# Performance work log

Hardware: AMD Instinct MI355X
Metric: run time of the kernel (lower is better)

Reference implementation:

```python
import jax, jax.numpy as jnp
import numpy as np

B, IN_DIM, HID, SUB_IN, SUB_OUT, GRID = 4096, 256, 512, 256, 256, 32
LN_EPS = 1e-5


def setup_inputs() -> dict:
    key = jax.random.key(0)
    ks = jax.random.split(key, 16)
    inp = {
        'x':  jax.random.normal(ks[0], (B, IN_DIM), jnp.float32),
        'h0': jax.random.normal(ks[1], (B, HID), jnp.float32),
        'c0': jax.random.normal(ks[2], (B, HID), jnp.float32),
        's0': jax.random.normal(ks[3], (B, SUB_OUT), jnp.float32),
        # LSTM gate params
        'kernel':  jax.random.normal(ks[4], (IN_DIM, 3 * HID), jnp.float32) * 0.05,
        'rkernel': jax.random.normal(ks[5], (HID, 3 * HID), jnp.float32) * 0.05,
        'bias':    jnp.zeros((3 * HID,), jnp.float32),
        # sub-layer recurrent mixing kernels (num_sub_layers=1)
        'sub_kx': jax.random.normal(ks[6], (1, IN_DIM, SUB_IN), jnp.float32) * 0.05,
        'sub_kh': jax.random.normal(ks[7], (1, SUB_OUT, SUB_IN), jnp.float32) * 0.05,
        'sub_tkan_kernel': jax.random.normal(ks[8], (1, 2 * SUB_OUT), jnp.float32) * 0.05,
        # Fourier KAN coefficients: (2, outdim, indim, gridsize) + bias
        'fc': jax.random.normal(ks[9], (2, SUB_OUT, SUB_IN, GRID), jnp.float32) / np.sqrt(SUB_IN * GRID),
        'fb': jnp.zeros((SUB_OUT,), jnp.float32),
        # aggregation + layer norm
        'agg_w': jax.random.normal(ks[10], (SUB_OUT, HID), jnp.float32) * 0.05,
        'agg_b': jnp.zeros((HID,), jnp.float32),
        'ln_g':  jnp.ones((HID,), jnp.float32),
        'ln_b':  jnp.zeros((HID,), jnp.float32),
    }
    return inp


def _fourier_kan(z, fc, fb):
    # z: [B, SUB_IN] -> [B, SUB_OUT]
    k = jnp.arange(1, GRID + 1, dtype=z.dtype)          # [G]
    ang = z[:, :, None] * k                             # [B, IN, G]
    return (jnp.einsum('big,oig->bo', jnp.cos(ang), fc[0])
            + jnp.einsum('big,oig->bo', jnp.sin(ang), fc[1]) + fb)


def reference(x, h0, c0, s0, kernel, rkernel, bias, sub_kx, sub_kh,
              sub_tkan_kernel, fc, fb, agg_w, agg_b, ln_g, ln_b):
    # LSTM-style gates (note: candidate also passes through sigmoid then tanh,
    # exactly as in the torch source)
    gates = jax.nn.sigmoid(x @ kernel + h0 @ rkernel + bias)      # [B, 3H]
    i, f, c_cand = jnp.split(gates, 3, axis=-1)
    c = f * c0 + i * jnp.tanh(c_cand)                             # [B, H]

    # single KAN sub-layer
    agg_in = x @ sub_kx[0] + s0 @ sub_kh[0]                       # [B, SUB_IN]
    sub_out = _fourier_kan(agg_in, fc, fb)                        # [B, SUB_OUT]
    rk_h, rk_x = jnp.split(sub_tkan_kernel[0], 2)                 # [SUB_OUT] each
    new_s = rk_h * sub_out + s0 * rk_x

    # aggregation -> output gate
    o = jax.nn.sigmoid(sub_out @ agg_w + agg_b)                   # [B, H]
    h = o * jnp.tanh(c)

    # layer norm
    mu = jnp.mean(h, axis=-1, keepdims=True)
    var = jnp.mean(jnp.square(h - mu), axis=-1, keepdims=True)
    h = (h - mu) * jax.lax.rsqrt(var + LN_EPS) * ln_g + ln_b
    return (h, c, new_s)
```

## Files before the change

kernel.cpp:

```cpp
#include <hip/hip_runtime.h>
#include <hip/hip_bf16.h>

typedef __bf16 bf16_t;
typedef __bf16 bf16x4 __attribute__((ext_vector_type(4)));
typedef __bf16 bf16x8 __attribute__((ext_vector_type(8)));
typedef float  f32x4  __attribute__((ext_vector_type(4)));

#define NB 4096
#define IN_DIM 256
#define HID 512
#define SUB 256
#define GRID_ 32

__device__ __forceinline__ float fract_f(float x) {
#if __has_builtin(__builtin_amdgcn_fractf)
  return __builtin_amdgcn_fractf(x);
#else
  return x - floorf(x);
#endif
}
__device__ __forceinline__ float cos_rev(float rev) {
#if __has_builtin(__builtin_amdgcn_cosf)
  return __builtin_amdgcn_cosf(rev);
#else
  return __cosf(rev * 6.283185307179586f);
#endif
}
__device__ __forceinline__ float sin_rev(float rev) {
#if __has_builtin(__builtin_amdgcn_sinf)
  return __builtin_amdgcn_sinf(rev);
#else
  return __sinf(rev * 6.283185307179586f);
#endif
}
__device__ __forceinline__ float sigm(float v) { return 1.f / (1.f + __expf(-v)); }
__device__ __forceinline__ float fast_tanh(float x) {
  float e = __expf(2.f * x);
  return (e - 1.f) / (e + 1.f);
}
#define INV2PI 0.15915494309189535f

#define O_XHI   0ull
#define O_XLO   2097152ull
#define O_H0    4194304ull
#define O_S0H   8388608ull
#define O_S0L   10485760ull
#define O_FCB   12582912ull
#define O_O     12582912ull
#define O_KT    20971520ull
#define O_RKT   21757952ull
#define O_AWT   23330816ull
#define O_KXH   23592960ull
#define O_KXL   23724032ull
#define O_KHH   23855104ull
#define O_KHL   23986176ull
#define O_TC    24117248ull
#define O_SOB   32505856ull
#define O_AGG   34603008ull
#define O_P3    38797312ull

__device__ __forceinline__ void tconv_body(const float* __restrict__ src,
                                           bf16_t* __restrict__ hi,
                                           bf16_t* __restrict__ lo,
                                           int R, int C, int bx, int by,
                                           bool wantlo, float scale) {
  __shared__ float t[32][33];
  int c0 = bx * 32, r0 = by * 32;
  int tx = threadIdx.x & 31, ty = threadIdx.x >> 5;
#pragma unroll
  for (int rr = 0; rr < 4; rr++) {
    int r = ty + rr * 8;
    t[r][tx] = src[(size_t)(r0 + r) * C + c0 + tx];
  }
  __syncthreads();
#pragma unroll
  for (int rr = 0; rr < 4; rr++) {
    int cl = ty + rr * 8;
    float f = t[tx][cl] * scale;
    bf16_t h = (bf16_t)f;
    size_t oi = (size_t)(c0 + cl) * R + r0 + tx;
    hi[oi] = h;
    if (wantlo) lo[oi] = (bf16_t)(f - (float)h);
  }
}

__global__ __launch_bounds__(256) void k_prep(const float* __restrict__ x,
                                              const float* __restrict__ h0,
                                              const float* __restrict__ s0,
                                              const float* __restrict__ fc,
                                              const float* __restrict__ Wk,
                                              const float* __restrict__ Wr,
                                              const float* __restrict__ aw,
                                              const float* __restrict__ kx,
                                              const float* __restrict__ kh,
                                              bf16_t* __restrict__ xhi, bf16_t* __restrict__ xlo,
                                              bf16_t* __restrict__ h0b,
                                              bf16_t* __restrict__ s0h, bf16_t* __restrict__ s0l,
                                              bf16_t* __restrict__ fcb2,
                                              bf16_t* __restrict__ kt,
                                              bf16_t* __restrict__ rkt,
                                              bf16_t* __restrict__ awt,
                                              bf16_t* __restrict__ kxh, bf16_t* __restrict__ kxl,
                                              bf16_t* __restrict__ khh, bf16_t* __restrict__ khl) {
  int bid = blockIdx.x;
  if (bid < 2048) {
    for (int q = bid * 256 + threadIdx.x; q < 2097152; q += 524288) {
      if (q < 1048576) {
        const float* src; bf16_t* hi; bf16_t* lo = nullptr; int base;
        if (q < 262144)       { src = x;  hi = xhi; lo = xlo; base = q; }
        else if (q < 786432)  { src = h0; hi = h0b;           base = q - 262144; }
        else                  { src = s0; hi = s0h; lo = s0l; base = q - 786432; }
        float4 v = *(const float4*)(src + (size_t)base * 4);
        bf16x4 h; h[0] = (bf16_t)v.x; h[1] = (bf16_t)v.y; h[2] = (bf16_t)v.z; h[3] = (bf16_t)v.w;
        *(bf16x4*)(hi + (size_t)base * 4) = h;
        if (lo) {
          bf16x4 l;
          l[0] = (bf16_t)(v.x - (float)h[0]); l[1] = (bf16_t)(v.y - (float)h[1]);
          l[2] = (bf16_t)(v.z - (float)h[2]); l[3] = (bf16_t)(v.w - (float)h[3]);
          *(bf16x4*)(lo + (size_t)base * 4) = l;
        }
      } else {
        int f = q - 1048576;
        int e = f * 4;
        int g = e & 31, i = (e >> 5) & 255, o = (e >> 13) & 255, s = e >> 21;
        float4 v = *(const float4*)(fc + (size_t)e);
        bf16x4 h; h[0] = (bf16_t)v.x; h[1] = (bf16_t)v.y; h[2] = (bf16_t)v.z; h[3] = (bf16_t)v.w;
        int nb = o >> 7, wn = (o >> 6) & 1, j = (o >> 4) & 3, lr = o & 15;
        int g4 = g >> 3, t0 = g & 7;
        size_t idx = ((((((size_t)(i * 2 + nb) * 2 + wn) * 4 + j) * 2 + s) * 4 + g4) * 16 + lr) * 8 + t0;
        *(bf16x4*)(fcb2 + idx) = h;
      }
    }
  } else {
    int b = bid - 2048;
    if (b < 384)       { tconv_body(Wk, kt,  nullptr, 256, 1536, b % 48, b / 48, false, 1.f); }
    else if (b < 1152) { b -= 384;  tconv_body(Wr, rkt, nullptr, 512, 1536, b % 48, b / 48, false, 1.f); }
    else if (b < 1280) { b -= 1152; tconv_body(aw, awt, nullptr, 256, 512,  b % 16, b / 16, false, 1.f); }
    else if (b < 1344) { b -= 1280; tconv_body(kx, kxh, kxl,     256, 256,  b % 8,  b / 8,  true, INV2PI); }
    else               { b -= 1344; tconv_body(kh, khh, khl,     256, 256,  b % 8,  b / 8,  true, INV2PI); }
  }
}

struct Pass { const bf16_t* A; const bf16_t* Bt; int K; int lda; int ldbt; };
struct GArgs {
  Pass p[6]; int np;
  const float* bias;
  int act;
  float* out; int ldout;
};

template<int BM, int BN>
__global__ __launch_bounds__(512) void k_gemm(GArgs g) {
  constexpr int MI = BM / 32;
  constexpr int NJ = BN / 64;
  constexpr int IA = (BM * 8) / 512;
  constexpr int IB = (BN * 8) / 512;
  __shared__ bf16_t smA[BM * 64];
  __shared__ bf16_t smB[BN * 64];
  const int tid = threadIdx.x;
  const int m0 = blockIdx.y * BM, n0 = blockIdx.x * BN;
  const int wv = tid >> 6, lane = tid & 63;
  const int wm = wv >> 2, wn = wv & 3;
  const int lr = lane & 15, g4 = lane >> 4;

  f32x4 acc[MI][NJ];
#pragma unroll
  for (int i = 0; i < MI; i++)
#pragma unroll
    for (int j = 0; j < NJ; j++) acc[i][j] = f32x4{0.f, 0.f, 0.f, 0.f};

  for (int ps = 0; ps < g.np; ps++) {
    const bf16_t* A = g.p[ps].A;
    const bf16_t* Bt = g.p[ps].Bt;
    const int K = g.p[ps].K, lda = g.p[ps].lda, ldbt = g.p[ps].ldbt;
    for (int k0 = 0; k0 < K; k0 += 64) {
      bf16x8 ar[IA], br[IB];
#pragma unroll
      for (int r = 0; r < IA; r++) {
        int task = tid + r * 512, row = task >> 3, t = task & 7, sf = t ^ (row & 7);
        ar[r] = *(const bf16x8*)(A + (size_t)(m0 + row) * lda + k0 + sf * 8);
      }
#pragma unroll
      for (int r = 0; r < IB; r++) {
        int task = tid + r * 512, row = task >> 3, t = task & 7, sf = t ^ (row & 7);
        br[r] = *(const bf16x8*)(Bt + (size_t)(n0 + row) * ldbt + k0 + sf * 8);
      }
      __syncthreads();
#pragma unroll
      for (int r = 0; r < IA; r++) {
        int task = tid + r * 512, row = task >> 3, t = task & 7;
        *(bf16x8*)(smA + row * 64 + t * 8) = ar[r];
      }
#pragma unroll
      for (int r = 0; r < IB; r++) {
        int task = tid + r * 512, row = task >> 3, t = task & 7;
        *(bf16x8*)(smB + row * 64 + t * 8) = br[r];
      }
      __syncthreads();
#pragma unroll
      for (int ks = 0; ks < 2; ks++) {
        bf16x8 af[MI], bfr[NJ];
#pragma unroll
        for (int i = 0; i < MI; i++) {
          int row = wm * (BM / 2) + i * 16 + lr;
          af[i] = *(const bf16x8*)(smA + row * 64 + ((ks * 4 + g4) ^ (lr & 7)) * 8);
        }
#pragma unroll
        for (int j = 0; j < NJ; j++) {
          int row = wn * (BN / 4) + j * 16 + lr;
          bfr[j] = *(const bf16x8*)(smB + row * 64 + ((ks * 4 + g4) ^ (lr & 7)) * 8);
        }
#pragma unroll
        for (int i = 0; i < MI; i++)
#pragma unroll
          for (int j = 0; j < NJ; j++)
            acc[i][j] = __builtin_amdgcn_mfma_f32_16x16x32_bf16(af[i], bfr[j], acc[i][j], 0, 0, 0);
      }
    }
  }
#pragma unroll
  for (int i = 0; i < MI; i++)
#pragma unroll
    for (int j = 0; j < NJ; j++) {
      int col = n0 + wn * (BN / 4) + j * 16 + lr;
      float bb = g.bias ? g.bias[col] : 0.f;
#pragma unroll
      for (int r = 0; r < 4; r++) {
        int row = m0 + wm * (BM / 2) + i * 16 + (lane >> 4) * 4 + r;
        float v = acc[i][j][r] + bb;
        if (g.act == 1) v = sigm(v);
        g.out[(size_t)row * g.ldout + col] = v;
      }
    }
}

struct GatesArgs {
  const bf16_t* xhi; const bf16_t* h0b; const bf16_t* kt; const bf16_t* rkt;
  const float* bias; const float* c0; float* c_out; float* tc;
};

__global__ __launch_bounds__(512, 2) void k_gates(GatesArgs ga) {
  __shared__ bf16_t smA[64 * 64];
  __shared__ bf16_t smB[3 * 128 * 64];
  const int tid = threadIdx.x;
  const int n0 = blockIdx.x * 128;
  const int m0 = blockIdx.y * 64;
  const int wv = tid >> 6, lane = tid & 63;
  const int wm = wv >> 2, wn = wv & 3;
  const int lr = lane & 15, g4 = lane >> 4;

  f32x4 acc[3][2][2];
#pragma unroll
  for (int t = 0; t < 3; t++)
#pragma unroll
    for (int i = 0; i < 2; i++)
#pragma unroll
      for (int j = 0; j < 2; j++) acc[t][i][j] = f32x4{0.f, 0.f, 0.f, 0.f};

  for (int ps = 0; ps < 2; ps++) {
    const bf16_t* A  = ps ? ga.h0b : ga.xhi;
    const bf16_t* Bt = ps ? ga.rkt : ga.kt;
    const int K = ps ? 512 : 256, ld = K;
    for (int k0 = 0; k0 < K; k0 += 64) {
      int arow = tid >> 3, at = tid & 7, asf = at ^ (arow & 7);
      bf16x8 ar = *(const bf16x8*)(A + (size_t)(m0 + arow) * ld + k0 + asf * 8);
      bf16x8 br[6];
#pragma unroll
      for (int r = 0; r < 6; r++) {
        int task = tid + r * 512;
        int gate = task >> 10, rem = task & 1023, o = rem >> 3, t = rem & 7, sf = t ^ (o & 7);
        br[r] = *(const bf16x8*)(Bt + (size_t)(gate * 512 + n0 + o) * ld + k0 + sf * 8);
      }
      __syncthreads();
      *(bf16x8*)(smA + arow * 64 + at * 8) = ar;
#pragma unroll
      for (int r = 0; r < 6; r++) {
        int task = tid + r * 512;
        int gate = task >> 10, rem = task & 1023, o = rem >> 3, t = rem & 7;
        *(bf16x8*)(smB + (gate * 128 + o) * 64 + t * 8) = br[r];
      }
      __syncthreads();
#pragma unroll
      for (int ks = 0; ks < 2; ks++) {
        bf16x8 af[2];
#pragma unroll
        for (int i = 0; i < 2; i++) {
          int row = wm * 32 + i * 16 + lr;
          af[i] = *(const bf16x8*)(smA + row * 64 + ((ks * 4 + g4) ^ (lr & 7)) * 8);
        }
#pragma unroll
        for (int t = 0; t < 3; t++) {
          bf16x8 bfr[2];
#pragma unroll
          for (int j = 0; j < 2; j++) {
            int row = wn * 32 + j * 16 + lr;
            bfr[j] = *(const bf16x8*)(smB + (t * 128 + row) * 64 + ((ks * 4 + g4) ^ (lr & 7)) * 8);
          }
#pragma unroll
          for (int i = 0; i < 2; i++)
#pragma unroll
            for (int j = 0; j < 2; j++)
              acc[t][i][j] = __builtin_amdgcn_mfma_f32_16x16x32_bf16(af[i], bfr[j], acc[t][i][j], 0, 0, 0);
        }
      }
    }
  }
#pragma unroll
  for (int i = 0; i < 2; i++)
#pragma unroll
    for (int j = 0; j < 2; j++) {
      int col = n0 + wn * 32 + j * 16 + lr;
      float bi = ga.bias[col], bf_ = ga.bias[512 + col], bc = ga.bias[1024 + col];
#pragma unroll
      for (int r = 0; r < 4; r++) {
        int row = m0 + wm * 32 + i * 16 + (lane >> 4) * 4 + r;
        size_t idx = (size_t)row * 512 + col;
        float iv = sigm(acc[0][i][j][r] + bi);
        float fv = sigm(acc[1][i][j][r] + bf_);
        float cc = sigm(acc[2][i][j][r] + bc);
        float cv = fv * ga.c0[idx] + iv * fast_tanh(cc);
        ga.c_out[idx] = cv;
        ga.tc[idx] = fast_tanh(cv);
      }
    }
}

struct FArgs { const float* agg; const bf16_t* fcb2; float* P[8]; };

__global__ __launch_bounds__(256, 2) void k_fourier(FArgs fa) {
  __shared__ float  zl[128 * 33];
  __shared__ bf16_t Asm[2][128 * 64];
  const int tid = threadIdx.x;
  const int bx = blockIdx.x;
  const int q = bx & 7, nb = (bx >> 3) & 1, mb = bx >> 4;
  const int m0 = mb * 128, n0 = nb * 128, i0 = q * 32;
  const int wv = tid >> 6, lane = tid & 63;
  const int wm = wv >> 1, wn = wv & 1;
  const int lr = lane & 15, g4 = lane >> 4;

#pragma unroll
  for (int r = 0; r < 4; r++) {
    int task = tid + r * 256, row = task >> 3, seg = task & 7;
    float4 v = *(const float4*)(fa.agg + (size_t)(m0 + row) * 256 + i0 + seg * 4);
    zl[row * 33 + seg * 4 + 0] = v.x;
    zl[row * 33 + seg * 4 + 1] = v.y;
    zl[row * 33 + seg * 4 + 2] = v.z;
    zl[row * 33 + seg * 4 + 3] = v.w;
  }

  const bf16_t* pB = fa.fcb2 + (size_t)i0 * 16384 + nb * 8192 + wn * 4096 + lane * 8;
  auto loadB = [&](int i, bf16x8 (&b)[8]) {
#pragma unroll
    for (int ks = 0; ks < 2; ks++)
#pragma unroll
      for (int j = 0; j < 4; j++)
        b[ks * 4 + j] = *(const bf16x8*)(pB + (size_t)i * 16384 + j * 1024 + ks * 512);
  };

  const int grow = tid >> 1, hp = tid & 1;
  const float* zp = zl + grow * 33;
  const int as0 = grow * 64 + (((2 * hp    ) ^ (grow & 7)) * 8);
  const int as1 = grow * 64 + (((2 * hp + 1) ^ (grow & 7)) * 8);
  const int as2 = grow * 64 + (((4 + 2 * hp) ^ (grow & 7)) * 8);
  const int as3 = grow * 64 + (((5 + 2 * hp) ^ (grow & 7)) * 8);
  auto genA = [&](int i, bf16_t* Ab) {
    float zr = zp[i];
    bf16x8 c0v, c1v, s0v, s1v;
#pragma unroll
    for (int t = 0; t < 8; t++) {
      float r0 = fract_f(zr * (float)(hp * 16 + t + 1));
      float r1 = fract_f(zr * (float)(hp * 16 + 8 + t + 1));
      c0v[t] = (bf16_t)cos_rev(r0); s0v[t] = (bf16_t)sin_rev(r0);
      c1v[t] = (bf16_t)cos_rev(r1); s1v[t] = (bf16_t)sin_rev(r1);
    }
    *(bf16x8*)(Ab + as0) = c0v;
    *(bf16x8*)(Ab + as1) = c1v;
    *(bf16x8*)(Ab + as2) = s0v;
    *(bf16x8*)(Ab + as3) = s1v;
  };

  int offA[8];
#pragma unroll
  for (int ks = 0; ks < 2; ks++)
#pragma unroll
    for (int i4 = 0; i4 < 4; i4++)
      offA[ks * 4 + i4] = (wm * 64 + i4 * 16 + lr) * 64 + ((ks * 4 + g4) ^ (lr & 7)) * 8;

  f32x4 acc[4][4];
#pragma unroll
  for (int i = 0; i < 4; i++)
#pragma unroll
    for (int j = 0; j < 4; j++) acc[i][j] = f32x4{0.f, 0.f, 0.f, 0.f};

  auto domfma = [&](const bf16x8 (&af)[8], const bf16x8 (&b)[8]) {
    __builtin_amdgcn_s_setprio(1);
#pragma unroll
    for (int ks = 0; ks < 2; ks++)
#pragma unroll
      for (int i4 = 0; i4 < 4; i4++)
#pragma unroll
        for (int j = 0; j < 4; j++)
          acc[i4][j] = __builtin_amdgcn_mfma_f32_16x16x32_bf16(af[ks * 4 + i4], b[ks * 4 + j], acc[i4][j], 0, 0, 0);
    __builtin_amdgcn_s_setprio(0);
  };
  auto readA = [&](const bf16_t* Ac, bf16x8 (&af)[8]) {
#pragma unroll
    for (int t = 0; t < 8; t++) af[t] = *(const bf16x8*)(Ac + offA[t]);
  };

  bf16x8 bA_[8], bB_[8];
  __syncthreads();
  loadB(0, bA_);
  genA(0, Asm[0]);
  asm volatile("s_waitcnt lgkmcnt(0)" ::: "memory");
  __builtin_amdgcn_s_barrier();

#pragma unroll 1
  for (int it = 0; it < 16; it++) {
    const int i = it * 2;
    bf16x8 af[8];
    if (i < 31) loadB(i + 1, bB_);
    readA(Asm[0], af);
    if (i < 31) genA(i + 1, Asm[1]);
    domfma(af, bA_);
    asm volatile("s_waitcnt lgkmcnt(0)" ::: "memory");
    __builtin_amdgcn_s_barrier();
    if (i + 2 < 32) loadB(i + 2, bA_);
    readA(Asm[1], af);
    if (i + 2 < 32) genA(i + 2, Asm[0]);
    domfma(af, bB_);
    asm volatile("s_waitcnt lgkmcnt(0)" ::: "memory");
    __builtin_amdgcn_s_barrier();
  }

  float* outp = fa.P[q];
#pragma unroll
  for (int i = 0; i < 4; i++)
#pragma unroll
    for (int j = 0; j < 4; j++) {
      int col = n0 + wn * 64 + j * 16 + lr;
#pragma unroll
      for (int r = 0; r < 4; r++) {
        int row = m0 + wm * 64 + i * 16 + g4 * 4 + r;
        outp[(size_t)row * 256 + col] = acc[i][j][r];
      }
    }
}

struct RArgs {
  const float* P[8];
  const float* fb; const float* tk; const float* s0;
  float* news; bf16_t* sob;
};

__global__ __launch_bounds__(256) void k_freduce(RArgs ra) {
  int stride = gridDim.x * blockDim.x;
  for (int qd = blockIdx.x * blockDim.x + threadIdx.x; qd < 262144; qd += stride) {
    int i = qd * 4, o = i & 255;
    float4 v = *(const float4*)(ra.P[0] + i);
#pragma unroll
    for (int c = 1; c < 8; c++) {
      float4 p = *(const float4*)(ra.P[c] + i);
      v.x += p.x; v.y += p.y; v.z += p.z; v.w += p.w;
    }
    v.x += ra.fb[o + 0]; v.y += ra.fb[o + 1]; v.z += ra.fb[o + 2]; v.w += ra.fb[o + 3];
    bf16x4 sb; sb[0] = (bf16_t)v.x; sb[1] = (bf16_t)v.y; sb[2] = (bf16_t)v.z; sb[3] = (bf16_t)v.w;
    *(bf16x4*)(ra.sob + i) = sb;
    float4 s = *(const float4*)(ra.s0 + i);
    float4 ns;
    ns.x = ra.tk[o + 0] * v.x + ra.tk[256 + o + 0] * s.x;
    ns.y = ra.tk[o + 1] * v.y + ra.tk[256 + o + 1] * s.y;
    ns.z = ra.tk[o + 2] * v.z + ra.tk[256 + o + 2] * s.z;
    ns.w = ra.tk[o + 3] * v.w + ra.tk[256 + o + 3] * s.w;
    *(float4*)(ra.news + i) = ns;
  }
}

__global__ __launch_bounds__(256) void k_ln(const float* __restrict__ o,
                                            const float* __restrict__ tc,
                                            const float* __restrict__ lg,
                                            const float* __restrict__ lb,
                                            float* __restrict__ h) {
  int b = blockIdx.x, tid = threadIdx.x;
  float2 ov = *(const float2*)(o + (size_t)b * 512 + tid * 2);
  float2 tv = *(const float2*)(tc + (size_t)b * 512 + tid * 2);
  float h0 = ov.x * tv.x, h1 = ov.y * tv.y;
  float s = h0 + h1, ss = h0 * h0 + h1 * h1;
#pragma unroll
  for (int off = 32; off; off >>= 1) {
    s += __shfl_xor(s, off);
    ss += __shfl_xor(ss, off);
  }
  __shared__ float red[8];
  int wid = tid >> 6;
  if ((tid & 63) == 0) { red[wid] = s; red[4 + wid] = ss; }
  __syncthreads();
  s = red[0] + red[1] + red[2] + red[3];
  ss = red[4] + red[5] + red[6] + red[7];
  float mu = s * (1.f / 512.f);
  float var = ss * (1.f / 512.f) - mu * mu;
  float rs = rsqrtf(var + 1e-5f);
  int j = tid * 2;
  h[(size_t)b * 512 + j]     = (h0 - mu) * rs * lg[j]     + lb[j];
  h[(size_t)b * 512 + j + 1] = (h1 - mu) * rs * lg[j + 1] + lb[j + 1];
}

extern "C" void kernel_launch(void* const* d_in, const int* in_sizes, int n_in,
                              void* d_out, int out_size, void* d_ws, size_t ws_size,
                              hipStream_t stream) {
  const float* x    = (const float*)d_in[0];
  const float* h0   = (const float*)d_in[1];
  const float* c0   = (const float*)d_in[2];
  const float* s0   = (const float*)d_in[3];
  const float* Wk   = (const float*)d_in[4];
  const float* Wr   = (const float*)d_in[5];
  const float* bias = (const float*)d_in[6];
  const float* kx   = (const float*)d_in[7];
  const float* kh   = (const float*)d_in[8];
  const float* tk   = (const float*)d_in[9];
  const float* fc   = (const float*)d_in[10];
  const float* fb   = (const float*)d_in[11];
  const float* aw   = (const float*)d_in[12];
  const float* ab   = (const float*)d_in[13];
  const float* lg   = (const float*)d_in[14];
  const float* lbp  = (const float*)d_in[15];
  float* out = (float*)d_out;
  char* ws = (char*)d_ws;
  auto BF = [&](unsigned long long off) { return (bf16_t*)(ws + off); };
  auto FP = [&](unsigned long long off) { return (float*)(ws + off); };

  k_prep<<<3456, 256, 0, stream>>>(x, h0, s0, fc, Wk, Wr, aw, kx, kh,
                                   BF(O_XHI), BF(O_XLO), BF(O_H0),
                                   BF(O_S0H), BF(O_S0L), BF(O_FCB),
                                   BF(O_KT), BF(O_RKT), BF(O_AWT),
                                   BF(O_KXH), BF(O_KXL), BF(O_KHH), BF(O_KHL));

  {
    GatesArgs ga{ BF(O_XHI), BF(O_H0), BF(O_KT), BF(O_RKT), bias, c0,
                  out + 2097152, FP(O_TC) };
    k_gates<<<dim3(4, 64), 512, 0, stream>>>(ga);
  }

  {
    GArgs g{};
    g.p[0] = { BF(O_XHI), BF(O_KXH), 256, 256, 256 };
    g.p[1] = { BF(O_XHI), BF(O_KXL), 256, 256, 256 };
    g.p[2] = { BF(O_XLO), BF(O_KXH), 256, 256, 256 };
    g.p[3] = { BF(O_S0H), BF(O_KHH), 256, 256, 256 };
    g.p[4] = { BF(O_S0H), BF(O_KHL), 256, 256, 256 };
    g.p[5] = { BF(O_S0L), BF(O_KHH), 256, 256, 256 };
    g.np = 6; g.bias = nullptr; g.act = 0;
    g.out = FP(O_AGG); g.ldout = 256;
    k_gemm<64, 64><<<dim3(4, 64), 512, 0, stream>>>(g);
  }

  FArgs fa;
  fa.agg = FP(O_AGG); fa.fcb2 = BF(O_FCB);
  fa.P[0] = FP(0ull);
  fa.P[1] = FP(4194304ull);
  fa.P[2] = FP(8388608ull);
  for (int c = 3; c < 8; c++) fa.P[c] = FP(O_P3 + (unsigned long long)(c - 3) * 4194304ull);
  k_fourier<<<512, 256, 0, stream>>>(fa);

  RArgs ra;
  for (int c = 0; c < 8; c++) ra.P[c] = fa.P[c];
  ra.fb = fb; ra.tk = tk; ra.s0 = s0;
  ra.news = out + 4194304; ra.sob = BF(O_SOB);
  k_freduce<<<1024, 256, 0, stream>>>(ra);

  {
    GArgs g{};
    g.p[0] = { BF(O_SOB), BF(O_AWT), 256, 256, 256 };
    g.np = 1; g.bias = ab; g.act = 1;
    g.out = FP(O_O); g.ldout = 512;
    k_gemm<64, 128><<<dim3(4, 64), 512, 0, stream>>>(g);
  }
  k_ln<<<4096, 256, 0, stream>>>(FP(O_O), FP(O_TC), lg, lbp, out);
}
```

Baseline: 115.0 us.

## Fuse aggregation GEMM with sigmoid and LayerNorm; shrink Fourier tile rows

Replaces the separate aggregation GEMM and the LayerNorm kernel with one kernel. Each block computes a full 64x512 row tile, applies the sigmoid and the tanh(c) product, and reduces mean and variance in registers and shared memory before writing h. This removes the intermediate o buffer round-trip and one launch, but only 64 blocks are launched, so occupancy on a large GPU is low and the B tile is reloaded without double buffering. The Fourier kernel is also retiled to 64-row blocks of 128 threads, giving 1024 blocks.

```diff
diff --git a/kernel.cpp b/kernel.cpp
--- a/kernel.cpp
+++ b/kernel.cpp
@@ -46,7 +46,6 @@
 #define O_S0H   8388608ull
 #define O_S0L   10485760ull
 #define O_FCB   12582912ull
-#define O_O     12582912ull
 #define O_KT    20971520ull
 #define O_RKT   21757952ull
 #define O_AWT   23330816ull
@@ -327,20 +326,20 @@
 
 struct FArgs { const float* agg; const bf16_t* fcb2; float* P[8]; };
 
-__global__ __launch_bounds__(256, 2) void k_fourier(FArgs fa) {
-  __shared__ float  zl[128 * 33];
-  __shared__ bf16_t Asm[2][128 * 64];
+__global__ __launch_bounds__(128, 2) void k_fourier(FArgs fa) {
+  __shared__ float  zl[64 * 33];
+  __shared__ bf16_t Asm[2][64 * 64];
   const int tid = threadIdx.x;
   const int bx = blockIdx.x;
   const int q = bx & 7, nb = (bx >> 3) & 1, mb = bx >> 4;
-  const int m0 = mb * 128, n0 = nb * 128, i0 = q * 32;
+  const int m0 = mb * 64, n0 = nb * 128, i0 = q * 32;
   const int wv = tid >> 6, lane = tid & 63;
-  const int wm = wv >> 1, wn = wv & 1;
+  const int wn = wv;
   const int lr = lane & 15, g4 = lane >> 4;
 
 #pragma unroll
   for (int r = 0; r < 4; r++) {
-    int task = tid + r * 256, row = task >> 3, seg = task & 7;
+    int task = tid + r * 128, row = task >> 3, seg = task & 7;
     float4 v = *(const float4*)(fa.agg + (size_t)(m0 + row) * 256 + i0 + seg * 4);
     zl[row * 33 + seg * 4 + 0] = v.x;
     zl[row * 33 + seg * 4 + 1] = v.y;
@@ -384,7 +383,7 @@
   for (int ks = 0; ks < 2; ks++)
 #pragma unroll
     for (int i4 = 0; i4 < 4; i4++)
-      offA[ks * 4 + i4] = (wm * 64 + i4 * 16 + lr) * 64 + ((ks * 4 + g4) ^ (lr & 7)) * 8;
+      offA[ks * 4 + i4] = (i4 * 16 + lr) * 64 + ((ks * 4 + g4) ^ (lr & 7)) * 8;
 
   f32x4 acc[4][4];
 #pragma unroll
@@ -441,7 +440,7 @@
       int col = n0 + wn * 64 + j * 16 + lr;
 #pragma unroll
       for (int r = 0; r < 4; r++) {
-        int row = m0 + wm * 64 + i * 16 + g4 * 4 + r;
+        int row = m0 + i * 16 + g4 * 4 + r;
         outp[(size_t)row * 256 + col] = acc[i][j][r];
       }
     }
@@ -476,33 +475,107 @@
   }
 }
 
-__global__ __launch_bounds__(256) void k_ln(const float* __restrict__ o,
-                                            const float* __restrict__ tc,
-                                            const float* __restrict__ lg,
-                                            const float* __restrict__ lb,
-                                            float* __restrict__ h) {
-  int b = blockIdx.x, tid = threadIdx.x;
-  float2 ov = *(const float2*)(o + (size_t)b * 512 + tid * 2);
-  float2 tv = *(const float2*)(tc + (size_t)b * 512 + tid * 2);
-  float h0 = ov.x * tv.x, h1 = ov.y * tv.y;
-  float s = h0 + h1, ss = h0 * h0 + h1 * h1;
-#pragma unroll
-  for (int off = 32; off; off >>= 1) {
-    s += __shfl_xor(s, off);
-    ss += __shfl_xor(ss, off);
-  }
-  __shared__ float red[8];
-  int wid = tid >> 6;
-  if ((tid & 63) == 0) { red[wid] = s; red[4 + wid] = ss; }
+struct OLArgs {
+  const bf16_t* sob; const bf16_t* awt; const float* ab;
+  const float* tc; const float* lg; const float* lb;
+  float* h;
+};
+
+__global__ __launch_bounds__(512) void k_oln(OLArgs a) {
+  __shared__ bf16_t smA[64 * 64];
+  __shared__ bf16_t smB[512 * 64];
+  __shared__ float redS[64][4], redSS[64][4];
+  const int tid = threadIdx.x;
+  const int m0 = blockIdx.x * 64;
+  const int wv = tid >> 6, lane = tid & 63;
+  const int wm = wv >> 2, wn = wv & 3;
+  const int lr = lane & 15, g4 = lane >> 4;
+
+  f32x4 acc[2][8];
+#pragma unroll
+  for (int i = 0; i < 2; i++)
+#pragma unroll
+    for (int j = 0; j < 8; j++) acc[i][j] = f32x4{0.f, 0.f, 0.f, 0.f};
+
+  for (int k0 = 0; k0 < 256; k0 += 64) {
+    int arow = tid >> 3, at = tid & 7, asf = at ^ (arow & 7);
+    bf16x8 ar = *(const bf16x8*)(a.sob + (size_t)(m0 + arow) * 256 + k0 + asf * 8);
+    bf16x8 br[8];
+#pragma unroll
+    for (int r = 0; r < 8; r++) {
+      int task = tid + r * 512, row = task >> 3, t = task & 7, sf = t ^ (row & 7);
+      br[r] = *(const bf16x8*)(a.awt + (size_t)row * 256 + k0 + sf * 8);
+    }
+    __syncthreads();
+    *(bf16x8*)(smA + arow * 64 + at * 8) = ar;
+#pragma unroll
+    for (int r = 0; r < 8; r++) {
+      int task = tid + r * 512, row = task >> 3, t = task & 7;
+      *(bf16x8*)(smB + row * 64 + t * 8) = br[r];
+    }
+    __syncthreads();
+#pragma unroll
+    for (int ks = 0; ks < 2; ks++) {
+      bf16x8 af[2], bfr[8];
+#pragma unroll
+      for (int i = 0; i < 2; i++) {
+        int row = wm * 32 + i * 16 + lr;
+        af[i] = *(const bf16x8*)(smA + row * 64 + ((ks * 4 + g4) ^ (lr & 7)) * 8);
+      }
+#pragma unroll
+      for (int j = 0; j < 8; j++) {
+        int row = wn * 128 + j * 16 + lr;
+        bfr[j] = *(const bf16x8*)(smB + row * 64 + ((ks * 4 + g4) ^ (lr & 7)) * 8);
+      }
+#pragma unroll
+      for (int i = 0; i < 2; i++)
+#pragma unroll
+        for (int j = 0; j < 8; j++)
+          acc[i][j] = __builtin_amdgcn_mfma_f32_16x16x32_bf16(af[i], bfr[j], acc[i][j], 0, 0, 0);
+    }
+  }
+
+#pragma unroll
+  for (int i = 0; i < 2; i++) {
+#pragma unroll
+    for (int r = 0; r < 4; r++) {
+      int rowL = wm * 32 + i * 16 + g4 * 4 + r;
+      int row = m0 + rowL;
+      float s = 0.f, ss = 0.f;
+#pragma unroll
+      for (int j = 0; j < 8; j++) {
+        int col = wn * 128 + j * 16 + lr;
+        float ov = sigm(acc[i][j][r] + a.ab[col]);
+        float hv = ov * a.tc[(size_t)row * 512 + col];
+        acc[i][j][r] = hv;
+        s += hv; ss += hv * hv;
+      }
+#pragma unroll
+      for (int off = 1; off < 16; off <<= 1) {
+        s += __shfl_xor(s, off);
+        ss += __shfl_xor(ss, off);
+      }
+      if (lr == 0) { redS[rowL][wn] = s; redSS[rowL][wn] = ss; }
+    }
+  }
   __syncthreads();
-  s = red[0] + red[1] + red[2] + red[3];
-  ss = red[4] + red[5] + red[6] + red[7];
-  float mu = s * (1.f / 512.f);
-  float var = ss * (1.f / 512.f) - mu * mu;
-  float rs = rsqrtf(var + 1e-5f);
-  int j = tid * 2;
-  h[(size_t)b * 512 + j]     = (h0 - mu) * rs * lg[j]     + lb[j];
-  h[(size_t)b * 512 + j + 1] = (h1 - mu) * rs * lg[j + 1] + lb[j + 1];
+#pragma unroll
+  for (int i = 0; i < 2; i++)
+#pragma unroll
+    for (int r = 0; r < 4; r++) {
+      int rowL = wm * 32 + i * 16 + g4 * 4 + r;
+      int row = m0 + rowL;
+      float S  = redS[rowL][0] + redS[rowL][1] + redS[rowL][2] + redS[rowL][3];
+      float SS = redSS[rowL][0] + redSS[rowL][1] + redSS[rowL][2] + redSS[rowL][3];
+      float mu = S * (1.f / 512.f);
+      float var = SS * (1.f / 512.f) - mu * mu;
+      float rs = rsqrtf(var + 1e-5f);
+#pragma unroll
+      for (int j = 0; j < 8; j++) {
+        int col = wn * 128 + j * 16 + lr;
+        a.h[(size_t)row * 512 + col] = (acc[i][j][r] - mu) * rs * a.lg[col] + a.lb[col];
+      }
+    }
 }
 
 extern "C" void kernel_launch(void* const* d_in, const int* in_sizes, int n_in,
@@ -560,7 +633,7 @@
   fa.P[1] = FP(4194304ull);
   fa.P[2] = FP(8388608ull);
   for (int c = 3; c < 8; c++) fa.P[c] = FP(O_P3 + (unsigned long long)(c - 3) * 4194304ull);
-  k_fourier<<<512, 256, 0, stream>>>(fa);
+  k_fourier<<<1024, 128, 0, stream>>>(fa);
 
   RArgs ra;
   for (int c = 0; c < 8; c++) ra.P[c] = fa.P[c];
@@ -569,11 +642,7 @@
   k_freduce<<<1024, 256, 0, stream>>>(ra);
 
   {
-    GArgs g{};
-    g.p[0] = { BF(O_SOB), BF(O_AWT), 256, 256, 256 };
-    g.np = 1; g.bias = ab; g.act = 1;
-    g.out = FP(O_O); g.ldout = 512;
-    k_gemm<64, 128><<<dim3(4, 64), 512, 0, stream>>>(g);
-  }
-  k_ln<<<4096, 256, 0, stream>>>(FP(O_O), FP(O_TC), lg, lbp, out);
-}
+    OLArgs oa{ BF(O_SOB), BF(O_AWT), ab, FP(O_TC), lg, lbp, out };
+    k_oln<<<64, 512, 0, stream>>>(oa);
+  }
+}
```

Result: slower. 124.0 us (+7.8%).

## Halve gates and Fourier block tiles and store intermediates in bf16

Applied to the files above, without the earlier changes.

The gates kernel moves to 256-thread blocks with 64-column tiles, and the Fourier kernel to 128-thread blocks with 64-row tiles. Both double the grid so more blocks are in flight across the CUs. The tanh(c) and output-gate intermediates are now written and read as bf16 instead of fp32, which halves their memory traffic into the layer-norm kernel. In exchange, each block gets less operand reuse per tile, and rounding those intermediates to bf16 lowers the precision of the normalized output.

```diff
diff --git a/kernel.cpp b/kernel.cpp
--- a/kernel.cpp
+++ b/kernel.cpp
@@ -2,6 +2,7 @@
 #include <hip/hip_bf16.h>
 
 typedef __bf16 bf16_t;
+typedef __bf16 bf16x2 __attribute__((ext_vector_type(2)));
 typedef __bf16 bf16x4 __attribute__((ext_vector_type(4)));
 typedef __bf16 bf16x8 __attribute__((ext_vector_type(8)));
 typedef float  f32x4  __attribute__((ext_vector_type(4)));
@@ -146,7 +147,7 @@
   Pass p[6]; int np;
   const float* bias;
   int act;
-  float* out; int ldout;
+  float* out; bf16_t* outb; int ldout;
 };
 
 template<int BM, int BN>
@@ -229,24 +230,25 @@
         int row = m0 + wm * (BM / 2) + i * 16 + (lane >> 4) * 4 + r;
         float v = acc[i][j][r] + bb;
         if (g.act == 1) v = sigm(v);
-        g.out[(size_t)row * g.ldout + col] = v;
+        if (g.outb) g.outb[(size_t)row * g.ldout + col] = (bf16_t)v;
+        else        g.out [(size_t)row * g.ldout + col] = v;
       }
     }
 }
 
 struct GatesArgs {
   const bf16_t* xhi; const bf16_t* h0b; const bf16_t* kt; const bf16_t* rkt;
-  const float* bias; const float* c0; float* c_out; float* tc;
+  const float* bias; const float* c0; float* c_out; bf16_t* tc;
 };
 
-__global__ __launch_bounds__(512, 2) void k_gates(GatesArgs ga) {
+__global__ __launch_bounds__(256, 2) void k_gates(GatesArgs ga) {
   __shared__ bf16_t smA[64 * 64];
-  __shared__ bf16_t smB[3 * 128 * 64];
+  __shared__ bf16_t smB[3 * 64 * 64];
   const int tid = threadIdx.x;
-  const int n0 = blockIdx.x * 128;
+  const int n0 = blockIdx.x * 64;
   const int m0 = blockIdx.y * 64;
   const int wv = tid >> 6, lane = tid & 63;
-  const int wm = wv >> 2, wn = wv & 3;
+  const int wm = wv >> 1, wn = wv & 1;
   const int lr = lane & 15, g4 = lane >> 4;
 
   f32x4 acc[3][2][2];
@@ -262,22 +264,29 @@
     const bf16_t* Bt = ps ? ga.rkt : ga.kt;
     const int K = ps ? 512 : 256, ld = K;
     for (int k0 = 0; k0 < K; k0 += 64) {
-      int arow = tid >> 3, at = tid & 7, asf = at ^ (arow & 7);
-      bf16x8 ar = *(const bf16x8*)(A + (size_t)(m0 + arow) * ld + k0 + asf * 8);
-      bf16x8 br[6];
+      bf16x8 ar[2], br[6];
+#pragma unroll
+      for (int r = 0; r < 2; r++) {
+        int task = tid + r * 256, row = task >> 3, t = task & 7, sf = t ^ (row & 7);
+        ar[r] = *(const bf16x8*)(A + (size_t)(m0 + row) * ld + k0 + sf * 8);
+      }
 #pragma unroll
       for (int r = 0; r < 6; r++) {
-        int task = tid + r * 512;
-        int gate = task >> 10, rem = task & 1023, o = rem >> 3, t = rem & 7, sf = t ^ (o & 7);
+        int task = tid + r * 256;
+        int gate = task >> 9, rem = task & 511, o = rem >> 3, t = rem & 7, sf = t ^ (o & 7);
         br[r] = *(const bf16x8*)(Bt + (size_t)(gate * 512 + n0 + o) * ld + k0 + sf * 8);
       }
       __syncthreads();
-      *(bf16x8*)(smA + arow * 64 + at * 8) = ar;
+#pragma unroll
+      for (int r = 0; r < 2; r++) {
+        int task = tid + r * 256, row = task >> 3, t = task & 7;
+        *(bf16x8*)(smA + row * 64 + t * 8) = ar[r];
+      }
 #pragma unroll
       for (int r = 0; r < 6; r++) {
-        int task = tid + r * 512;
-        int gate = task >> 10, rem = task & 1023, o = rem >> 3, t = rem & 7;
-        *(bf16x8*)(smB + (gate * 128 + o) * 64 + t * 8) = br[r];
+        int task = tid + r * 256;
+        int gate = task >> 9, rem = task & 511, o = rem >> 3, t = rem & 7;
+        *(bf16x8*)(smB + (gate * 64 + o) * 64 + t * 8) = br[r];
       }
       __syncthreads();
 #pragma unroll
@@ -294,7 +303,7 @@
 #pragma unroll
           for (int j = 0; j < 2; j++) {
             int row = wn * 32 + j * 16 + lr;
-            bfr[j] = *(const bf16x8*)(smB + (t * 128 + row) * 64 + ((ks * 4 + g4) ^ (lr & 7)) * 8);
+            bfr[j] = *(const bf16x8*)(smB + (t * 64 + row) * 64 + ((ks * 4 + g4) ^ (lr & 7)) * 8);
           }
 #pragma unroll
           for (int i = 0; i < 2; i++)
@@ -313,34 +322,34 @@
       float bi = ga.bias[col], bf_ = ga.bias[512 + col], bc = ga.bias[1024 + col];
 #pragma unroll
       for (int r = 0; r < 4; r++) {
-        int row = m0 + wm * 32 + i * 16 + (lane >> 4) * 4 + r;
+        int row = m0 + wm * 32 + i * 16 + g4 * 4 + r;
         size_t idx = (size_t)row * 512 + col;
         float iv = sigm(acc[0][i][j][r] + bi);
         float fv = sigm(acc[1][i][j][r] + bf_);
         float cc = sigm(acc[2][i][j][r] + bc);
         float cv = fv * ga.c0[idx] + iv * fast_tanh(cc);
         ga.c_out[idx] = cv;
-        ga.tc[idx] = fast_tanh(cv);
+        ga.tc[idx] = (bf16_t)fast_tanh(cv);
       }
     }
 }
 
 struct FArgs { const float* agg; const bf16_t* fcb2; float* P[8]; };
 
-__global__ __launch_bounds__(256, 2) void k_fourier(FArgs fa) {
-  __shared__ float  zl[128 * 33];
-  __shared__ bf16_t Asm[2][128 * 64];
+__global__ __launch_bounds__(128, 2) void k_fourier(FArgs fa) {
+  __shared__ float  zl[64 * 33];
+  __shared__ bf16_t Asm[2][64 * 64];
   const int tid = threadIdx.x;
   const int bx = blockIdx.x;
   const int q = bx & 7, nb = (bx >> 3) & 1, mb = bx >> 4;
-  const int m0 = mb * 128, n0 = nb * 128, i0 = q * 32;
+  const int m0 = mb * 64, n0 = nb * 128, i0 = q * 32;
   const int wv = tid >> 6, lane = tid & 63;
-  const int wm = wv >> 1, wn = wv & 1;
+  const int wn = wv;
   const int lr = lane & 15, g4 = lane >> 4;
 
 #pragma unroll
   for (int r = 0; r < 4; r++) {
-    int task = tid + r * 256, row = task >> 3, seg = task & 7;
+    int task = tid + r * 128, row = task >> 3, seg = task & 7;
     float4 v = *(const float4*)(fa.agg + (size_t)(m0 + row) * 256 + i0 + seg * 4);
     zl[row * 33 + seg * 4 + 0] = v.x;
     zl[row * 33 + seg * 4 + 1] = v.y;
@@ -384,7 +393,7 @@
   for (int ks = 0; ks < 2; ks++)
 #pragma unroll
     for (int i4 = 0; i4 < 4; i4++)
-      offA[ks * 4 + i4] = (wm * 64 + i4 * 16 + lr) * 64 + ((ks * 4 + g4) ^ (lr & 7)) * 8;
+      offA[ks * 4 + i4] = (i4 * 16 + lr) * 64 + ((ks * 4 + g4) ^ (lr & 7)) * 8;
 
   f32x4 acc[4][4];
 #pragma unroll
@@ -441,7 +450,7 @@
       int col = n0 + wn * 64 + j * 16 + lr;
 #pragma unroll
       for (int r = 0; r < 4; r++) {
-        int row = m0 + wm * 64 + i * 16 + g4 * 4 + r;
+        int row = m0 + i * 16 + g4 * 4 + r;
         outp[(size_t)row * 256 + col] = acc[i][j][r];
       }
     }
@@ -476,15 +485,15 @@
   }
 }
 
-__global__ __launch_bounds__(256) void k_ln(const float* __restrict__ o,
-                                            const float* __restrict__ tc,
+__global__ __launch_bounds__(256) void k_ln(const bf16_t* __restrict__ o,
+                                            const bf16_t* __restrict__ tc,
                                             const float* __restrict__ lg,
                                             const float* __restrict__ lb,
                                             float* __restrict__ h) {
   int b = blockIdx.x, tid = threadIdx.x;
-  float2 ov = *(const float2*)(o + (size_t)b * 512 + tid * 2);
-  float2 tv = *(const float2*)(tc + (size_t)b * 512 + tid * 2);
-  float h0 = ov.x * tv.x, h1 = ov.y * tv.y;
+  bf16x2 ov = *(const bf16x2*)(o + (size_t)b * 512 + tid * 2);
+  bf16x2 tv = *(const bf16x2*)(tc + (size_t)b * 512 + tid * 2);
+  float h0 = (float)ov[0] * (float)tv[0], h1 = (float)ov[1] * (float)tv[1];
   float s = h0 + h1, ss = h0 * h0 + h1 * h1;
 #pragma unroll
   for (int off = 32; off; off >>= 1) {
@@ -537,8 +546,8 @@
 
   {
     GatesArgs ga{ BF(O_XHI), BF(O_H0), BF(O_KT), BF(O_RKT), bias, c0,
-                  out + 2097152, FP(O_TC) };
-    k_gates<<<dim3(4, 64), 512, 0, stream>>>(ga);
+                  out + 2097152, BF(O_TC) };
+    k_gates<<<dim3(8, 64), 256, 0, stream>>>(ga);
   }
 
   {
@@ -550,7 +559,7 @@
     g.p[4] = { BF(O_S0H), BF(O_KHL), 256, 256, 256 };
     g.p[5] = { BF(O_S0L), BF(O_KHH), 256, 256, 256 };
     g.np = 6; g.bias = nullptr; g.act = 0;
-    g.out = FP(O_AGG); g.ldout = 256;
+    g.out = FP(O_AGG); g.outb = nullptr; g.ldout = 256;
     k_gemm<64, 64><<<dim3(4, 64), 512, 0, stream>>>(g);
   }
 
@@ -560,7 +569,7 @@
   fa.P[1] = FP(4194304ull);
   fa.P[2] = FP(8388608ull);
   for (int c = 3; c < 8; c++) fa.P[c] = FP(O_P3 + (unsigned long long)(c - 3) * 4194304ull);
-  k_fourier<<<512, 256, 0, stream>>>(fa);
+  k_fourier<<<1024, 128, 0, stream>>>(fa);
 
   RArgs ra;
   for (int c = 0; c < 8; c++) ra.P[c] = fa.P[c];
@@ -572,8 +581,8 @@
     GArgs g{};
     g.p[0] = { BF(O_SOB), BF(O_AWT), 256, 256, 256 };
     g.np = 1; g.bias = ab; g.act = 1;
-    g.out = FP(O_O); g.ldout = 512;
+    g.out = nullptr; g.outb = BF(O_O); g.ldout = 512;
     k_gemm<64, 128><<<dim3(4, 64), 512, 0, stream>>>(g);
   }
-  k_ln<<<4096, 256, 0, stream>>>(FP(O_O), FP(O_TC), lg, lbp, out);
-}
+  k_ln<<<4096, 256, 0, stream>>>(BF(O_O), BF(O_TC), lg, lbp, out);
+}
```

New measurement: 113.7 us. No clear change (-1.1%).
